# Optimization experiments

Measured on AMD Instinct MI355X. Metric: run time of the kernel, lower is better.

Reference implementation:

```python
import jax, jax.numpy as jnp
import numpy as np

N, CIN, H, W = 8, 128, 56, 56
COUT, KH, KW = 128, 3, 3
STRIDE, PAD, DIL = 1, 1, 1
HO = (H + 2 * PAD - DIL * (KH - 1) - 1) // STRIDE + 1
WO = (W + 2 * PAD - DIL * (KW - 1) - 1) // STRIDE + 1
K = KH * KW


def setup_inputs() -> dict:
    key = jax.random.key(0)
    k1, k2, k3, k4, k5 = jax.random.split(key, 5)
    x = jax.random.normal(k1, (N, CIN, H, W), dtype=jnp.float32)
    offset = jax.random.normal(k2, (N, 2 * K, HO, WO), dtype=jnp.float32)
    weight = jax.random.normal(k3, (COUT, CIN, KH, KW), dtype=jnp.float32) * (1.0 / np.sqrt(CIN * K))
    bias = jax.random.normal(k4, (COUT,), dtype=jnp.float32) * 0.01
    x2 = jax.random.normal(k5, (N, COUT, HO, WO), dtype=jnp.float32)
    return {"x": x, "offset": offset, "weight": weight, "bias": bias, "x2": x2}


def _deform_conv2d(x, offset, weight, bias):
    n, c, h, w = x.shape
    cout = weight.shape[0]
    # offset layout (torchvision): channels = [dy_0, dx_0, dy_1, dx_1, ...]
    off = offset.reshape(n, K, 2, HO, WO)
    ki = jnp.arange(KH).repeat(KW)          # kernel row index per k   [K]
    kj = jnp.tile(jnp.arange(KW), KH)       # kernel col index per k   [K]
    base_y = (jnp.arange(HO) * STRIDE - PAD)[None, :, None] + (ki * DIL)[:, None, None]  # [K,HO,1]
    base_x = (jnp.arange(WO) * STRIDE - PAD)[None, None, :] + (kj * DIL)[:, None, None]  # [K,1,WO]
    py = base_y[None].astype(x.dtype) + off[:, :, 0]   # [N,K,HO,WO]
    px = base_x[None].astype(x.dtype) + off[:, :, 1]   # [N,K,HO,WO]

    y0 = jnp.floor(py).astype(jnp.int32)
    x0 = jnp.floor(px).astype(jnp.int32)
    wy = py - y0.astype(x.dtype)
    wx = px - x0.astype(x.dtype)

    xf = x.reshape(n, c, h * w)

    def gather(yi, xi):
        valid = (yi >= 0) & (yi < h) & (xi >= 0) & (xi < w)        # [N,K,HO,WO]
        lin = jnp.clip(yi, 0, h - 1) * w + jnp.clip(xi, 0, w - 1)  # [N,K,HO,WO]
        v = jax.vmap(lambda xfn, idx: xfn[:, idx])(xf, lin)        # [N,C,K,HO,WO]
        return v * valid[:, None].astype(x.dtype)

    v00 = gather(y0, x0)
    v01 = gather(y0, x0 + 1)
    v10 = gather(y0 + 1, x0)
    v11 = gather(y0 + 1, x0 + 1)
    wy = wy[:, None]
    wx = wx[:, None]
    cols = (v00 * (1 - wy) * (1 - wx) + v01 * (1 - wy) * wx
            + v10 * wy * (1 - wx) + v11 * wy * wx)                 # [N,C,K,HO,WO]

    wmat = weight.reshape(cout, c, K)
    out = jnp.einsum('nckhw,ock->nohw', cols, wmat)
    return out + bias[None, :, None, None]


def reference(x, offset, weight, bias, x2):
    out = _deform_conv2d(x, offset, weight, bias)
    return jax.nn.relu(out + x2)
```

## Files before the change

### kernel.cpp

```cpp
#include <hip/hip_runtime.h>

#define N_IMG 8
#define CIN   128
#define H_IN  56
#define W_IN  56
#define COUT  128
#define HW    3136
#define TROWS 9
#define TILE_B (TROWS * 56 * 256)
#define PMC_OFF TILE_B
#define PMW_OFF (TILE_B + 4608)
#define SMEM_TOTAL (TILE_B + 4608 + 9216)

typedef __attribute__((ext_vector_type(8))) short short8;
typedef __attribute__((ext_vector_type(4))) float f32x4;
typedef _Float16 h8 __attribute__((ext_vector_type(8)));

__device__ __forceinline__ unsigned short hb(float f) {
    _Float16 h = (_Float16)f;
    return __builtin_bit_cast(unsigned short, h);
}
__device__ __forceinline__ h8 splat8(unsigned short b) {
    _Float16 s = __builtin_bit_cast(_Float16, b);
    return (h8){s, s, s, s, s, s, s, s};
}
__device__ __forceinline__ void gload16(const void* g, void* l) {
    __builtin_amdgcn_global_load_lds(
        (const __attribute__((address_space(1))) unsigned int*)g,
        (__attribute__((address_space(3))) unsigned int*)l, 16, 0, 0);
}

__global__ __launch_bounds__(256) void prep_kernel(const float* __restrict__ x,
                                                   const float* __restrict__ w,
                                                   unsigned short* __restrict__ xt,
                                                   unsigned short* __restrict__ wr) {
    int b = blockIdx.x;
    int tid = threadIdx.x;
    if (b < 784) {
        int c = tid & 127;
        int half = tid >> 7;
        int n = b / 98;
        int hw0 = (b - n * 98) * 32 + half * 16;
        const float* xp = x + ((size_t)(n * CIN + c)) * HW + hw0;
        unsigned short* op = xt + ((size_t)n * HW + hw0) * CIN + c;
#pragma unroll
        for (int r = 0; r < 16; ++r) op[r * CIN] = hb(xp[r]);
    } else {
        int G = (b - 784) * 256 + tid;
        int lane = G & 63;
        int f = (G >> 6) & 7;
        int kc4 = (G >> 9) & 3;
        int tap = G >> 11;
        int cout = f * 16 + (lane & 15);
        int ch = kc4 * 32 + (lane >> 4) * 8;
        short8 v;
#pragma unroll
        for (int j = 0; j < 8; ++j)
            v[j] = (short)hb(w[((size_t)cout * CIN + ch + j) * 9 + tap]);
        *(short8*)(wr + (size_t)G * 8) = v;
    }
}

__global__ __launch_bounds__(1024, 4) void deform_main(
    const float* __restrict__ offset, const float* __restrict__ x2,
    const float* __restrict__ bias, const unsigned short* __restrict__ xt,
    const unsigned short* __restrict__ wr, float* __restrict__ out)
{
    extern __shared__ char smem[];
    int*     pmc = (int*)(smem + PMC_OFF);
    ushort4* pmw = (ushort4*)(smem + PMW_OFF);

    int tid = threadIdx.x;
    int orig = blockIdx.x;
    int n   = orig & 7;
    int ro0 = (orig >> 3) * 2;

    const char* xim = (const char*)(xt + (size_t)n * HW * CIN);

#pragma unroll
    for (int s = 0; s < 8; ++s) {
        int d = s * 16384 + tid * 16;
        if (d < TILE_B) {
            int p = d >> 8;
            int tr = p / 56;
            int tx = p - tr * 56;
            int gy = min(max(ro0 - 3 + tr, 0), 55);
            int c  = ((d >> 4) & 15) ^ (p & 15);
            gload16(xim + (((gy * 56 + tx) << 8) + (c << 4)), smem + d);
        }
    }

    for (int e = tid; e < 1152; e += 1024) {
        int r = (e >= 576) ? 1 : 0;
        int e2 = e - r * 576;
        int tap = e2 >> 6;
        int px  = e2 & 63;
        int wo  = min(px, 55);
        int hor = ro0 + r;
        const float* offp = offset + ((size_t)n * 18 + tap * 2) * HW + hor * 56 + wo;
        float offy = offp[0];
        float offx = offp[HW];
        int ki = tap / 3;
        int kj = tap - ki * 3;
        float py  = (float)(hor - 1 + ki) + offy;
        float pxf = (float)(wo - 1 + kj) + offx;
        float y0f = floorf(py), x0f = floorf(pxf);
        float wy = py - y0f, wx = pxf - x0f;
        int y0 = (int)y0f, x0 = (int)x0f;
        int y1 = y0 + 1, x1 = x0 + 1;
        bool vy0 = (y0 >= 0) && (y0 < H_IN);
        bool vy1 = (y1 >= 0) && (y1 < H_IN);
        bool vx0 = (x0 >= 0) && (x0 < W_IN);
        bool vx1 = (x1 >= 0) && (x1 < W_IN);
        int cy0 = min(max(y0, 0), 55), cy1 = min(max(y1, 0), 55);
        int cx0 = min(max(x0, 0), 55), cx1 = min(max(x1, 0), 55);
        int f0 = (y0 < ro0 - 3 || y0 > ro0 + 5) ? 1 : 0;
        int f1 = (y1 < ro0 - 3 || y1 > ro0 + 5) ? 1 : 0;
        pmc[e] = cy0 | (cy1 << 6) | (cx0 << 12) | (cx1 << 18) | (f0 << 24) | (f1 << 25);
        ushort4 wp;
        wp.x = hb((vy0 && vx0) ? (1.f - wy) * (1.f - wx) : 0.f);
        wp.y = hb((vy0 && vx1) ? (1.f - wy) * wx : 0.f);
        wp.z = hb((vy1 && vx0) ? wy * (1.f - wx) : 0.f);
        wp.w = hb((vy1 && vx1) ? wy * wx : 0.f);
        pmw[e] = wp;
    }
    __syncthreads();

    int lane = tid & 63;
    int w16 = tid >> 6;
    int kg = w16 & 1;
    int mt = w16 >> 1;
    int llo = lane & 15, lhi = lane >> 4;
    int slot = mt * 16 + llo;
    int row = slot >> 6;
    int px  = slot & 63;
    int ebase = row * 576 + px;
    const char* wrb = (const char*)wr;

    f32x4 acc[8] = {};

    for (int tap = 0; tap < 9; ++tap) {
        int cw = pmc[ebase + tap * 64];
        ushort4 wp = pmw[ebase + tap * 64];
        int cy0 = cw & 63, cy1 = (cw >> 6) & 63;
        int cx0 = (cw >> 12) & 63, cx1 = (cw >> 18) & 63;
        int f0 = (cw >> 24) & 1, f1 = (cw >> 25) & 1;
        int tr0 = min(max(cy0 + 3 - ro0, 0), TROWS - 1);
        int tr1 = min(max(cy1 + 3 - ro0, 0), TROWS - 1);
        int p00 = tr0 * 56 + cx0, p01 = tr0 * 56 + cx1;
        int p10 = tr1 * 56 + cx0, p11 = tr1 * 56 + cx1;
        bool any_fb = __any((f0 & ((wp.x != 0) | (wp.y != 0))) |
                            (f1 & ((wp.z != 0) | (wp.w != 0))));

#pragma unroll
        for (int kc = 0; kc < 2; ++kc) {
            int cbase = kg * 8 + kc * 4 + lhi;
            h8 g0 = *(const h8*)(smem + (p00 << 8) + ((cbase ^ (p00 & 15)) << 4));
            h8 g1 = *(const h8*)(smem + (p01 << 8) + ((cbase ^ (p01 & 15)) << 4));
            h8 g2 = *(const h8*)(smem + (p10 << 8) + ((cbase ^ (p10 & 15)) << 4));
            h8 g3 = *(const h8*)(smem + (p11 << 8) + ((cbase ^ (p11 & 15)) << 4));
            if (any_fb) {
                if (f0 && (wp.x != 0)) g0 = *(const h8*)(xim + ((size_t)(cy0 * 56 + cx0) << 8) + (cbase << 4));
                if (f0 && (wp.y != 0)) g1 = *(const h8*)(xim + ((size_t)(cy0 * 56 + cx1) << 8) + (cbase << 4));
                if (f1 && (wp.z != 0)) g2 = *(const h8*)(xim + ((size_t)(cy1 * 56 + cx0) << 8) + (cbase << 4));
                if (f1 && (wp.w != 0)) g3 = *(const h8*)(xim + ((size_t)(cy1 * 56 + cx1) << 8) + (cbase << 4));
            }
            h8 a = g0 * splat8(wp.x) + g1 * splat8(wp.y)
                 + g2 * splat8(wp.z) + g3 * splat8(wp.w);

            const char* bb = wrb + (size_t)((tap * 4 + kg * 2 + kc) * 8) * 1024 + lane * 16;
#pragma unroll
            for (int f = 0; f < 8; ++f) {
                h8 bf = *(const h8*)(bb + f * 1024);
                acc[f] = __builtin_amdgcn_mfma_f32_16x16x32_f16(a, bf, acc[f], 0, 0, 0);
            }
        }
    }

    __syncthreads();
    if (kg == 1) {
#pragma unroll
        for (int f = 0; f < 8; ++f)
            *(f32x4*)(smem + (((mt * 8 + f) * 64 + lane) << 4)) = acc[f];
    }
    __syncthreads();
    if (kg == 0) {
#pragma unroll
        for (int f = 0; f < 8; ++f)
            acc[f] += *(const f32x4*)(smem + (((mt * 8 + f) * 64 + lane) << 4));

        int slotq = mt * 16 + lhi * 4;
        int srow = slotq >> 6;
        int wo4 = slotq & 63;
        if (wo4 < 56) {
#pragma unroll
            for (int f = 0; f < 8; ++f) {
                int cout = f * 16 + llo;
                float bb = bias[cout];
                size_t off = ((size_t)(n * COUT + cout)) * HW + (ro0 + srow) * 56 + wo4;
                f32x4 xv = *(const f32x4*)(x2 + off);
                f32x4 o;
#pragma unroll
                for (int r = 0; r < 4; ++r) {
                    float v = acc[f][r] + bb + xv[r];
                    o[r] = v > 0.f ? v : 0.f;
                }
                *(f32x4*)(out + off) = o;
            }
        }
    }
}

extern "C" void kernel_launch(void* const* d_in, const int* in_sizes, int n_in,
                              void* d_out, int out_size, void* d_ws, size_t ws_size,
                              hipStream_t stream) {
    const float* x      = (const float*)d_in[0];
    const float* offset = (const float*)d_in[1];
    const float* weight = (const float*)d_in[2];
    const float* bias   = (const float*)d_in[3];
    const float* x2     = (const float*)d_in[4];
    float* out = (float*)d_out;

    unsigned short* xt = (unsigned short*)d_ws;
    unsigned short* wr = (unsigned short*)((char*)d_ws + 6422528ULL);

    hipFuncSetAttribute((const void*)deform_main,
                        hipFuncAttributeMaxDynamicSharedMemorySize, SMEM_TOTAL);
    prep_kernel<<<856, 256, 0, stream>>>(x, weight, xt, wr);
    deform_main<<<224, 1024, SMEM_TOTAL, stream>>>(offset, x2, bias, xt, wr, out);
}
```

Baseline: 38.02 us.

## Split taps across three wave groups and share weight fragments over two M-tiles

Work inside each block is reorganised. Twelve waves replace sixteen, and each wave handles two 16-pixel M-tiles over a group of three taps and all 128 input channels, where before it handled one M-tile over half the channels of all taps. Each loaded weight B fragment now feeds two MFMAs, which halves global and L2 weight traffic per MFMA and frees issue slots. The cost is more registers (16 accumulators plus 8 prefetched B fragments), fewer waves to hide gather and LDS latency, and a larger three-way cross-group reduction through LDS.

```diff
diff --git a/kernel.cpp b/kernel.cpp
--- a/kernel.cpp
+++ b/kernel.cpp
@@ -61,7 +61,7 @@
     }
 }
 
-__global__ __launch_bounds__(1024, 4) void deform_main(
+__global__ __launch_bounds__(768, 3) void deform_main(
     const float* __restrict__ offset, const float* __restrict__ x2,
     const float* __restrict__ bias, const unsigned short* __restrict__ xt,
     const unsigned short* __restrict__ wr, float* __restrict__ out)
@@ -78,8 +78,8 @@
     const char* xim = (const char*)(xt + (size_t)n * HW * CIN);
 
 #pragma unroll
-    for (int s = 0; s < 8; ++s) {
-        int d = s * 16384 + tid * 16;
+    for (int s = 0; s < 11; ++s) {
+        int d = s * 12288 + tid * 16;
         if (d < TILE_B) {
             int p = d >> 8;
             int tr = p / 56;
@@ -90,7 +90,7 @@
         }
     }
 
-    for (int e = tid; e < 1152; e += 1024) {
+    for (int e = tid; e < 1152; e += 768) {
         int r = (e >= 576) ? 1 : 0;
         int e2 = e - r * 576;
         int tap = e2 >> 6;
@@ -127,85 +127,132 @@
     __syncthreads();
 
     int lane = tid & 63;
-    int w16 = tid >> 6;
-    int kg = w16 & 1;
-    int mt = w16 >> 1;
+    int w12 = tid >> 6;
+    int mt = w12 & 3;
+    int kg = w12 >> 2;
     int llo = lane & 15, lhi = lane >> 4;
-    int slot = mt * 16 + llo;
-    int row = slot >> 6;
-    int px  = slot & 63;
-    int ebase = row * 576 + px;
+    int slot0 = mt * 32 + llo;
+    int slot1 = slot0 + 16;
+    int eb0 = (slot0 >> 6) * 576 + (slot0 & 63);
+    int eb1 = (slot1 >> 6) * 576 + (slot1 & 63);
     const char* wrb = (const char*)wr;
 
-    f32x4 acc[8] = {};
-
-    for (int tap = 0; tap < 9; ++tap) {
-        int cw = pmc[ebase + tap * 64];
-        ushort4 wp = pmw[ebase + tap * 64];
-        int cy0 = cw & 63, cy1 = (cw >> 6) & 63;
-        int cx0 = (cw >> 12) & 63, cx1 = (cw >> 18) & 63;
-        int f0 = (cw >> 24) & 1, f1 = (cw >> 25) & 1;
-        int tr0 = min(max(cy0 + 3 - ro0, 0), TROWS - 1);
-        int tr1 = min(max(cy1 + 3 - ro0, 0), TROWS - 1);
-        int p00 = tr0 * 56 + cx0, p01 = tr0 * 56 + cx1;
-        int p10 = tr1 * 56 + cx0, p11 = tr1 * 56 + cx1;
-        bool any_fb = __any((f0 & ((wp.x != 0) | (wp.y != 0))) |
-                            (f1 & ((wp.z != 0) | (wp.w != 0))));
-
-#pragma unroll
-        for (int kc = 0; kc < 2; ++kc) {
-            int cbase = kg * 8 + kc * 4 + lhi;
-            h8 g0 = *(const h8*)(smem + (p00 << 8) + ((cbase ^ (p00 & 15)) << 4));
-            h8 g1 = *(const h8*)(smem + (p01 << 8) + ((cbase ^ (p01 & 15)) << 4));
-            h8 g2 = *(const h8*)(smem + (p10 << 8) + ((cbase ^ (p10 & 15)) << 4));
-            h8 g3 = *(const h8*)(smem + (p11 << 8) + ((cbase ^ (p11 & 15)) << 4));
-            if (any_fb) {
-                if (f0 && (wp.x != 0)) g0 = *(const h8*)(xim + ((size_t)(cy0 * 56 + cx0) << 8) + (cbase << 4));
-                if (f0 && (wp.y != 0)) g1 = *(const h8*)(xim + ((size_t)(cy0 * 56 + cx1) << 8) + (cbase << 4));
-                if (f1 && (wp.z != 0)) g2 = *(const h8*)(xim + ((size_t)(cy1 * 56 + cx0) << 8) + (cbase << 4));
-                if (f1 && (wp.w != 0)) g3 = *(const h8*)(xim + ((size_t)(cy1 * 56 + cx1) << 8) + (cbase << 4));
-            }
-            h8 a = g0 * splat8(wp.x) + g1 * splat8(wp.y)
-                 + g2 * splat8(wp.z) + g3 * splat8(wp.w);
-
-            const char* bb = wrb + (size_t)((tap * 4 + kg * 2 + kc) * 8) * 1024 + lane * 16;
+    f32x4 acc[2][8] = {};
+
+    for (int t3 = 0; t3 < 3; ++t3) {
+        int tap = kg * 3 + t3;
+        int cw0 = pmc[eb0 + tap * 64];
+        int cw1 = pmc[eb1 + tap * 64];
+        ushort4 wp0 = pmw[eb0 + tap * 64];
+        ushort4 wp1 = pmw[eb1 + tap * 64];
+        int a_cy0 = cw0 & 63, a_cy1 = (cw0 >> 6) & 63;
+        int a_cx0 = (cw0 >> 12) & 63, a_cx1 = (cw0 >> 18) & 63;
+        int a_tr0 = min(max(a_cy0 + 3 - ro0, 0), TROWS - 1);
+        int a_tr1 = min(max(a_cy1 + 3 - ro0, 0), TROWS - 1);
+        int a_p00 = a_tr0 * 56 + a_cx0, a_p01 = a_tr0 * 56 + a_cx1;
+        int a_p10 = a_tr1 * 56 + a_cx0, a_p11 = a_tr1 * 56 + a_cx1;
+        bool a_b0 = ((cw0 >> 24) & 1) && (wp0.x != 0);
+        bool a_b1 = ((cw0 >> 24) & 1) && (wp0.y != 0);
+        bool a_b2 = ((cw0 >> 25) & 1) && (wp0.z != 0);
+        bool a_b3 = ((cw0 >> 25) & 1) && (wp0.w != 0);
+        bool a_fb = __any(a_b0 | a_b1 | a_b2 | a_b3);
+        int c_cy0 = cw1 & 63, c_cy1 = (cw1 >> 6) & 63;
+        int c_cx0 = (cw1 >> 12) & 63, c_cx1 = (cw1 >> 18) & 63;
+        int c_tr0 = min(max(c_cy0 + 3 - ro0, 0), TROWS - 1);
+        int c_tr1 = min(max(c_cy1 + 3 - ro0, 0), TROWS - 1);
+        int c_p00 = c_tr0 * 56 + c_cx0, c_p01 = c_tr0 * 56 + c_cx1;
+        int c_p10 = c_tr1 * 56 + c_cx0, c_p11 = c_tr1 * 56 + c_cx1;
+        bool c_b0 = ((cw1 >> 24) & 1) && (wp1.x != 0);
+        bool c_b1 = ((cw1 >> 24) & 1) && (wp1.y != 0);
+        bool c_b2 = ((cw1 >> 25) & 1) && (wp1.z != 0);
+        bool c_b3 = ((cw1 >> 25) & 1) && (wp1.w != 0);
+        bool c_fb = __any(c_b0 | c_b1 | c_b2 | c_b3);
+
+        const char* bb = wrb + (size_t)tap * 32768 + lane * 16;
+
+#pragma unroll
+        for (int kc = 0; kc < 4; ++kc) {
+            h8 bf[8];
+#pragma unroll
+            for (int f = 0; f < 8; ++f)
+                bf[f] = *(const h8*)(bb + kc * 8192 + f * 1024);
+
+            int cbase = kc * 4 + lhi;
+
+            h8 g0 = *(const h8*)(smem + (a_p00 << 8) + ((cbase ^ (a_p00 & 15)) << 4));
+            h8 g1 = *(const h8*)(smem + (a_p01 << 8) + ((cbase ^ (a_p01 & 15)) << 4));
+            h8 g2 = *(const h8*)(smem + (a_p10 << 8) + ((cbase ^ (a_p10 & 15)) << 4));
+            h8 g3 = *(const h8*)(smem + (a_p11 << 8) + ((cbase ^ (a_p11 & 15)) << 4));
+            if (a_fb) {
+                if (a_b0) g0 = *(const h8*)(xim + ((size_t)(a_cy0 * 56 + a_cx0) << 8) + (cbase << 4));
+                if (a_b1) g1 = *(const h8*)(xim + ((size_t)(a_cy0 * 56 + a_cx1) << 8) + (cbase << 4));
+                if (a_b2) g2 = *(const h8*)(xim + ((size_t)(a_cy1 * 56 + a_cx0) << 8) + (cbase << 4));
+                if (a_b3) g3 = *(const h8*)(xim + ((size_t)(a_cy1 * 56 + a_cx1) << 8) + (cbase << 4));
+            }
+            h8 a0 = g0 * splat8(wp0.x) + g1 * splat8(wp0.y)
+                  + g2 * splat8(wp0.z) + g3 * splat8(wp0.w);
+
+            h8 h0 = *(const h8*)(smem + (c_p00 << 8) + ((cbase ^ (c_p00 & 15)) << 4));
+            h8 h1 = *(const h8*)(smem + (c_p01 << 8) + ((cbase ^ (c_p01 & 15)) << 4));
+            h8 h2 = *(const h8*)(smem + (c_p10 << 8) + ((cbase ^ (c_p10 & 15)) << 4));
+            h8 h3 = *(const h8*)(smem + (c_p11 << 8) + ((cbase ^ (c_p11 & 15)) << 4));
+            if (c_fb) {
+                if (c_b0) h0 = *(const h8*)(xim + ((size_t)(c_cy0 * 56 + c_cx0) << 8) + (cbase << 4));
+                if (c_b1) h1 = *(const h8*)(xim + ((size_t)(c_cy0 * 56 + c_cx1) << 8) + (cbase << 4));
+                if (c_b2) h2 = *(const h8*)(xim + ((size_t)(c_cy1 * 56 + c_cx0) << 8) + (cbase << 4));
+                if (c_b3) h3 = *(const h8*)(xim + ((size_t)(c_cy1 * 56 + c_cx1) << 8) + (cbase << 4));
+            }
+            h8 a1 = h0 * splat8(wp1.x) + h1 * splat8(wp1.y)
+                  + h2 * splat8(wp1.z) + h3 * splat8(wp1.w);
+
 #pragma unroll
             for (int f = 0; f < 8; ++f) {
-                h8 bf = *(const h8*)(bb + f * 1024);
-                acc[f] = __builtin_amdgcn_mfma_f32_16x16x32_f16(a, bf, acc[f], 0, 0, 0);
+                acc[0][f] = __builtin_amdgcn_mfma_f32_16x16x32_f16(a0, bf[f], acc[0][f], 0, 0, 0);
+                acc[1][f] = __builtin_amdgcn_mfma_f32_16x16x32_f16(a1, bf[f], acc[1][f], 0, 0, 0);
             }
         }
     }
 
     __syncthreads();
-    if (kg == 1) {
-#pragma unroll
-        for (int f = 0; f < 8; ++f)
-            *(f32x4*)(smem + (((mt * 8 + f) * 64 + lane) << 4)) = acc[f];
+    if (kg > 0) {
+        char* red = smem + (size_t)(kg - 1) * 65536;
+#pragma unroll
+        for (int q = 0; q < 2; ++q)
+#pragma unroll
+            for (int f = 0; f < 8; ++f)
+                *(f32x4*)(red + ((((mt * 2 + q) * 8 + f) << 10) + (lane << 4))) = acc[q][f];
     }
     __syncthreads();
     if (kg == 0) {
 #pragma unroll
-        for (int f = 0; f < 8; ++f)
-            acc[f] += *(const f32x4*)(smem + (((mt * 8 + f) * 64 + lane) << 4));
-
-        int slotq = mt * 16 + lhi * 4;
-        int srow = slotq >> 6;
-        int wo4 = slotq & 63;
-        if (wo4 < 56) {
+        for (int q = 0; q < 2; ++q)
 #pragma unroll
             for (int f = 0; f < 8; ++f) {
-                int cout = f * 16 + llo;
-                float bb = bias[cout];
-                size_t off = ((size_t)(n * COUT + cout)) * HW + (ro0 + srow) * 56 + wo4;
-                f32x4 xv = *(const f32x4*)(x2 + off);
-                f32x4 o;
-#pragma unroll
-                for (int r = 0; r < 4; ++r) {
-                    float v = acc[f][r] + bb + xv[r];
-                    o[r] = v > 0.f ? v : 0.f;
+                size_t ro = (((mt * 2 + q) * 8 + f) << 10) + (lane << 4);
+                acc[q][f] += *(const f32x4*)(smem + ro);
+                acc[q][f] += *(const f32x4*)(smem + 65536 + ro);
+            }
+
+#pragma unroll
+        for (int q = 0; q < 2; ++q) {
+            int slotq = mt * 32 + q * 16 + lhi * 4;
+            int srow = slotq >> 6;
+            int wo4 = slotq & 63;
+            if (wo4 < 56) {
+#pragma unroll
+                for (int f = 0; f < 8; ++f) {
+                    int cout = f * 16 + llo;
+                    float bb = bias[cout];
+                    size_t off = ((size_t)(n * COUT + cout)) * HW + (ro0 + srow) * 56 + wo4;
+                    f32x4 xv = *(const f32x4*)(x2 + off);
+                    f32x4 o;
+#pragma unroll
+                    for (int r = 0; r < 4; ++r) {
+                        float v = acc[q][f][r] + bb + xv[r];
+                        o[r] = v > 0.f ? v : 0.f;
+                    }
+                    *(f32x4*)(out + off) = o;
                 }
-                *(f32x4*)(out + off) = o;
             }
         }
     }
@@ -227,5 +274,5 @@
     hipFuncSetAttribute((const void*)deform_main,
                         hipFuncAttributeMaxDynamicSharedMemorySize, SMEM_TOTAL);
     prep_kernel<<<856, 256, 0, stream>>>(x, weight, xt, wr);
-    deform_main<<<224, 1024, SMEM_TOTAL, stream>>>(offset, x2, bias, xt, wr, out);
-}
+    deform_main<<<224, 768, SMEM_TOTAL, stream>>>(offset, x2, bias, xt, wr, out);
+}
```

New measurement: 39.11 us. +2.9%, slower.
